# Kernel tuning notes

Measured on AMD Instinct MI355X. Metric: run time of the kernel, lower is better.

## Reference

```python
import jax, jax.numpy as jnp
import numpy as np

B, L, HID, NH = 2, 2048, 1024, 16
HD = HID // NH  # 64


def setup_inputs() -> dict:
    key = jax.random.key(0)
    ks = jax.random.split(key, 12)
    s = 1.0 / np.sqrt(HID)
    query = jax.random.normal(ks[0], (B, L, HID), jnp.float32)
    key_t = jax.random.normal(ks[1], (B, L, HID), jnp.float32)
    value = jax.random.normal(ks[2], (B, L, HID), jnp.float32)
    # key padding mask: True = valid token; random lengths in [1024, 2048]
    lengths = jax.random.randint(ks[3], (B,), L // 2, L + 1)
    key_mask = jnp.arange(L)[None, :] < lengths[:, None]  # [B, K] bool
    # attn_mask: True = blocked (causal upper triangle), 2D branch [Q, K]
    attn_mask = jnp.triu(jnp.ones((L, L), jnp.bool_), k=1)
    Wq = jax.random.normal(ks[4], (HID, HID), jnp.float32) * s
    Wk = jax.random.normal(ks[5], (HID, HID), jnp.float32) * s
    Wv = jax.random.normal(ks[6], (HID, HID), jnp.float32) * s
    Wo = jax.random.normal(ks[7], (HID, HID), jnp.float32) * s
    bq = jax.random.normal(ks[8], (HID,), jnp.float32) * 0.01
    bk = jax.random.normal(ks[9], (HID,), jnp.float32) * 0.01
    bv = jax.random.normal(ks[10], (HID,), jnp.float32) * 0.01
    bo = jax.random.normal(ks[11], (HID,), jnp.float32) * 0.01
    return {"query": query, "key": key_t, "value": value,
            "key_mask": key_mask, "attn_mask": attn_mask,
            "Wq": Wq, "bq": bq, "Wk": Wk, "bk": bk,
            "Wv": Wv, "bv": bv, "Wo": Wo, "bo": bo}


def reference(query, key, value, key_mask, attn_mask,
              Wq, bq, Wk, bk, Wv, bv, Wo, bo):
    Bq, Q, _ = query.shape
    K = key.shape[1]
    # projections (torch Linear: x @ W.T + b), split heads -> [B, H, L, HD]
    def proj(x, W, b, L_):
        return (x @ W.T + b).reshape(Bq, L_, NH, HD).transpose(0, 2, 1, 3)
    q = proj(query, Wq, bq, Q)
    k = proj(key, Wk, bk, K)
    v = proj(value, Wv, bv, K)
    scores = jnp.einsum('bhqd,bhkd->bhqk', q, k) / np.sqrt(HD)
    blocked = attn_mask[None, None, :, :]                 # True = blocked
    kmask = key_mask[:, None, None, :]                    # True = valid
    valid = (~blocked) & kmask                            # [B,H,Q,K] (bcast)
    scores = jnp.where(blocked, -10000.0, scores)
    scores = jnp.where(kmask, scores, -10000.0)
    weights = jax.nn.softmax(scores, axis=-1)
    weights = weights * valid.astype(weights.dtype)
    weights = weights / jnp.maximum(weights.sum(-1, keepdims=True), 1e-6)
    attended = jnp.einsum('bhqk,bhkd->bhqd', weights, v)
    attended = attended.transpose(0, 2, 1, 3).reshape(Bq, Q, HID)
    return attended @ Wo.T + bo
```

## Files before the change

### kernel.cpp

```cpp
#include <hip/hip_runtime.h>
#include <hip/hip_bf16.h>
#include <stdint.h>


#define L_SEQ 2048
#define HID 1024
#define NHEAD 16
#define HD 64

typedef __attribute__((ext_vector_type(8))) short bf16x8;
typedef __attribute__((ext_vector_type(8))) unsigned short u16x8;
typedef __attribute__((ext_vector_type(4))) float f32x4;

__device__ __forceinline__ unsigned short f2bf(float f) {
  unsigned int u = __builtin_bit_cast(unsigned int, f);
  u += 0x7fffu + ((u >> 16) & 1u);
  return (unsigned short)(u >> 16);
}

__device__ __forceinline__ unsigned int pk2bf(float a, float b) {
  unsigned int r;
  asm("v_cvt_pk_bf16_f32 %0, %1, %2" : "=v"(r) : "v"(a), "v"(b));
  return r;
}

__device__ __forceinline__ void gl_lds16(const void* g, void* l) {
  __builtin_amdgcn_global_load_lds(
      (const __attribute__((address_space(1))) unsigned int*)(uintptr_t)g,
      (__attribute__((address_space(3))) unsigned int*)(uint32_t)(uintptr_t)l,
      16, 0, 0);
}

__device__ __forceinline__ f32x4 mfma16(bf16x8 a, bf16x8 b, f32x4 c) {
  return __builtin_amdgcn_mfma_f32_16x16x32_bf16(a, b, c, 0, 0, 0);
}

__global__ __launch_bounds__(256)
void convert_w_kernel(const float* __restrict__ wq, const float* __restrict__ wk,
                      const float* __restrict__ wv, const float* __restrict__ wo,
                      const unsigned int* __restrict__ km,
                      unsigned short* __restrict__ wqb, unsigned short* __restrict__ wkb,
                      unsigned short* __restrict__ wvb, unsigned short* __restrict__ wob,
                      int* __restrict__ lens) {
  __shared__ int red[256];
  const int bid = blockIdx.x;
  const int t = threadIdx.x;
  if (bid == 2048) {
    unsigned int w0 = km[0];
    bool u8mode = (w0 != 1u);
    for (int b = 0; b < 2; ++b) {
      int cnt = 0;
      if (u8mode) {
        const unsigned char* p = (const unsigned char*)km + b * L_SEQ;
        for (int i = t; i < L_SEQ; i += 256) cnt += (p[i] != 0) ? 1 : 0;
      } else {
        const unsigned int* p = km + b * L_SEQ;
        for (int i = t; i < L_SEQ; i += 256) cnt += (p[i] != 0) ? 1 : 0;
      }
      red[t] = cnt;
      __syncthreads();
      for (int s = 128; s > 0; s >>= 1) {
        if (t < s) red[t] += red[t + s];
        __syncthreads();
      }
      if (t == 0) lens[b] = red[0];
      __syncthreads();
    }
    return;
  }
  int s = bid >> 9;
  int base = (bid & 511) * 2048;
  const float* src = s == 0 ? wq : (s == 1 ? wk : (s == 2 ? wv : wo));
  unsigned short* dst = s == 0 ? wqb : (s == 1 ? wkb : (s == 2 ? wvb : wob));
  int i = base + t * 8;
  float4 a = *(const float4*)(src + i);
  float4 b4 = *(const float4*)(src + i + 4);
  u16x8 o;
  o[0] = f2bf(a.x); o[1] = f2bf(a.y); o[2] = f2bf(a.z); o[3] = f2bf(a.w);
  o[4] = f2bf(b4.x); o[5] = f2bf(b4.y); o[6] = f2bf(b4.z); o[7] = f2bf(b4.w);
  *(u16x8*)(dst + i) = o;
}

__device__ __forceinline__ void gemm128_f32A_core(const float* __restrict__ A,
                                                  const unsigned short* __restrict__ W,
                                                  int m0, int n0, int K,
                                                  unsigned short* As, unsigned short* Bs,
                                                  f32x4 acc[4][4]) {
  const int tid = threadIdx.x;
  const int w = tid >> 6, lane = tid & 63;
  const int l15 = lane & 15, l4 = lane >> 4;
  const int wr = w >> 1, wc = w & 1;
#pragma unroll
  for (int i = 0; i < 4; ++i)
#pragma unroll
    for (int j = 0; j < 4; ++j) acc[i][j] = (f32x4){0.f, 0.f, 0.f, 0.f};

  const int arow = tid >> 1, acolh = (tid & 1) * 16;
  const float* Ag = A + (size_t)(m0 + arow) * K + acolh;
  char* AsW = (char*)As + arow * 64 + acolh * 2;
  const int nk = K >> 5;

  {
    float4 a0 = *(const float4*)(Ag);
    float4 a1 = *(const float4*)(Ag + 4);
    float4 a2 = *(const float4*)(Ag + 8);
    float4 a3 = *(const float4*)(Ag + 12);
    uint4 p0, p1;
    p0.x = pk2bf(a0.x, a0.y); p0.y = pk2bf(a0.z, a0.w);
    p0.z = pk2bf(a1.x, a1.y); p0.w = pk2bf(a1.z, a1.w);
    p1.x = pk2bf(a2.x, a2.y); p1.y = pk2bf(a2.z, a2.w);
    p1.z = pk2bf(a3.x, a3.y); p1.w = pk2bf(a3.z, a3.w);
    *(uint4*)(AsW) = p0;
    *(uint4*)(AsW + 16) = p1;
#pragma unroll
    for (int i = 0; i < 2; ++i) {
      int c = i * 256 + tid;
      int row = c >> 2, col = (c & 3) * 8;
      gl_lds16(W + (size_t)(n0 + row) * K + col, (char*)Bs + (i * 256 + w * 64) * 16);
    }
  }
  __syncthreads();

  int cur = 0;
  for (int t = 0; t < nk; ++t) {
    const int k0 = t * 32;
    float4 a0, a1, a2, a3;
    const bool more = (t + 1 < nk);
    if (more) {
      const float* Agn = Ag + k0 + 32;
      a0 = *(const float4*)(Agn);
      a1 = *(const float4*)(Agn + 4);
      a2 = *(const float4*)(Agn + 8);
      a3 = *(const float4*)(Agn + 12);
#pragma unroll
      for (int i = 0; i < 2; ++i) {
        int c = i * 256 + tid;
        int row = c >> 2, col = (c & 3) * 8;
        gl_lds16(W + (size_t)(n0 + row) * K + k0 + 32 + col,
                 (char*)Bs + (cur ^ 1) * 8192 + (i * 256 + w * 64) * 16);
      }
    }
    const unsigned short* Asb = As + cur * 4096;
    const unsigned short* Bsb = Bs + cur * 4096;
    bf16x8 af[4], bfr[4];
#pragma unroll
    for (int i = 0; i < 4; ++i)
      af[i] = *(const bf16x8*)(Asb + (wr * 64 + i * 16 + l15) * 32 + l4 * 8);
#pragma unroll
    for (int j = 0; j < 4; ++j)
      bfr[j] = *(const bf16x8*)(Bsb + (wc * 64 + j * 16 + l15) * 32 + l4 * 8);
    __builtin_amdgcn_s_setprio(1);
#pragma unroll
    for (int i = 0; i < 4; ++i)
#pragma unroll
      for (int j = 0; j < 4; ++j) acc[i][j] = mfma16(af[i], bfr[j], acc[i][j]);
    __builtin_amdgcn_s_setprio(0);
    if (more) {
      uint4 p0, p1;
      p0.x = pk2bf(a0.x, a0.y); p0.y = pk2bf(a0.z, a0.w);
      p0.z = pk2bf(a1.x, a1.y); p0.w = pk2bf(a1.z, a1.w);
      p1.x = pk2bf(a2.x, a2.y); p1.y = pk2bf(a2.z, a2.w);
      p1.z = pk2bf(a3.x, a3.y); p1.w = pk2bf(a3.z, a3.w);
      char* dst = AsW + (cur ^ 1) * 8192;
      *(uint4*)(dst) = p0;
      *(uint4*)(dst + 16) = p1;
    }
    __syncthreads();
    cur ^= 1;
  }
}

__device__ __forceinline__ void gemm128_bf_core(const unsigned short* __restrict__ A,
                                                const unsigned short* __restrict__ W,
                                                int m0, int n0, int K,
                                                unsigned short* As, unsigned short* Bs,
                                                f32x4 acc[4][4]) {
  const int tid = threadIdx.x;
  const int w = tid >> 6, lane = tid & 63;
  const int l15 = lane & 15, l4 = lane >> 4;
  const int wr = w >> 1, wc = w & 1;
#pragma unroll
  for (int i = 0; i < 4; ++i)
#pragma unroll
    for (int j = 0; j < 4; ++j) acc[i][j] = (f32x4){0.f, 0.f, 0.f, 0.f};

  const int nk = K >> 5;
#pragma unroll
  for (int i = 0; i < 2; ++i) {
    int c = i * 256 + tid;
    int row = c >> 2, col = (c & 3) * 8;
    gl_lds16(A + (size_t)(m0 + row) * K + col, (char*)As + (i * 256 + w * 64) * 16);
    gl_lds16(W + (size_t)(n0 + row) * K + col, (char*)Bs + (i * 256 + w * 64) * 16);
  }
  __syncthreads();

  int cur = 0;
  for (int t = 0; t < nk; ++t) {
    const int k0 = t * 32;
    if (t + 1 < nk) {
#pragma unroll
      for (int i = 0; i < 2; ++i) {
        int c = i * 256 + tid;
        int row = c >> 2, col = (c & 3) * 8;
        gl_lds16(A + (size_t)(m0 + row) * K + k0 + 32 + col,
                 (char*)As + (cur ^ 1) * 8192 + (i * 256 + w * 64) * 16);
        gl_lds16(W + (size_t)(n0 + row) * K + k0 + 32 + col,
                 (char*)Bs + (cur ^ 1) * 8192 + (i * 256 + w * 64) * 16);
      }
    }
    const unsigned short* Asb = As + cur * 4096;
    const unsigned short* Bsb = Bs + cur * 4096;
    bf16x8 af[4], bfr[4];
#pragma unroll
    for (int i = 0; i < 4; ++i)
      af[i] = *(const bf16x8*)(Asb + (wr * 64 + i * 16 + l15) * 32 + l4 * 8);
#pragma unroll
    for (int j = 0; j < 4; ++j)
      bfr[j] = *(const bf16x8*)(Bsb + (wc * 64 + j * 16 + l15) * 32 + l4 * 8);
    __builtin_amdgcn_s_setprio(1);
#pragma unroll
    for (int i = 0; i < 4; ++i)
#pragma unroll
      for (int j = 0; j < 4; ++j) acc[i][j] = mfma16(af[i], bfr[j], acc[i][j]);
    __builtin_amdgcn_s_setprio(0);
    __syncthreads();
    cur ^= 1;
  }
}

__global__ __launch_bounds__(256)
void qkv_gemm_kernel(const float* __restrict__ qf32, const float* __restrict__ kf32,
                     const float* __restrict__ vf32, const unsigned short* __restrict__ wq,
                     const unsigned short* __restrict__ wk, const unsigned short* __restrict__ wv,
                     const float* __restrict__ bq, const float* __restrict__ bk,
                     const float* __restrict__ bv, unsigned short* __restrict__ Qp,
                     unsigned short* __restrict__ Kp, unsigned short* __restrict__ Vtp) {
  __shared__ unsigned short As[2 * 128 * 32];
  __shared__ unsigned short Bs[2 * 128 * 32];
  const int z = blockIdx.z;
  const float* A = z == 0 ? qf32 : (z == 1 ? kf32 : vf32);
  const unsigned short* W = z == 0 ? wq : (z == 1 ? wk : wv);
  const float* bias = z == 0 ? bq : (z == 1 ? bk : bv);
  const int m0 = blockIdx.y * 128, n0 = blockIdx.x * 128;
  f32x4 acc[4][4];
  gemm128_f32A_core(A, W, m0, n0, HID, As, Bs, acc);

  const int tid = threadIdx.x;
  const int w = tid >> 6, lane = tid & 63;
  const int l15 = lane & 15, l4 = lane >> 4;
  const int wr = w >> 1, wc = w & 1;
  const float scale = (z == 0) ? 0.125f * 1.44269504089f : 1.0f;
  if (z == 2) {
#pragma unroll
    for (int i = 0; i < 4; ++i)
#pragma unroll
      for (int j = 0; j < 4; ++j) {
        int grow0 = m0 + wr * 64 + i * 16 + l4 * 4;
        int gcol = n0 + wc * 64 + j * 16 + l15;
        float bv_ = bias[gcol];
        int bb = grow0 >> 11, ll0 = grow0 & 2047;
        int hh = gcol >> 6, d = gcol & 63;
        uint2 pw;
        pw.x = pk2bf(acc[i][j][0] + bv_, acc[i][j][1] + bv_);
        pw.y = pk2bf(acc[i][j][2] + bv_, acc[i][j][3] + bv_);
        *(uint2*)(&Vtp[((size_t)(bb * NHEAD + hh) * HD + d) * L_SEQ + ll0]) = pw;
      }
  } else {
    unsigned short* P = (z == 0) ? Qp : Kp;
#pragma unroll
    for (int i = 0; i < 4; ++i)
#pragma unroll
      for (int j = 0; j < 4; ++j)
#pragma unroll
        for (int r = 0; r < 4; ++r) {
          int grow = m0 + wr * 64 + i * 16 + l4 * 4 + r;
          int gcol = n0 + wc * 64 + j * 16 + l15;
          float v = (acc[i][j][r] + bias[gcol]) * scale;
          int bb = grow >> 11, ll = grow & 2047;
          int hh = gcol >> 6, d = gcol & 63;
          P[((size_t)(bb * NHEAD + hh) * L_SEQ + ll) * HD + d] = f2bf(v);
        }
  }
}

__global__ __launch_bounds__(256)
void out_gemm_kernel(const unsigned short* __restrict__ att, const unsigned short* __restrict__ wo,
                     const float* __restrict__ bo, float* __restrict__ out) {
  __shared__ unsigned short As[2 * 128 * 32];
  __shared__ unsigned short Bs[2 * 128 * 32];
  const int m0 = blockIdx.y * 128, n0 = blockIdx.x * 128;
  f32x4 acc[4][4];
  gemm128_bf_core(att, wo, m0, n0, HID, As, Bs, acc);

  const int tid = threadIdx.x;
  const int w = tid >> 6, lane = tid & 63;
  const int l15 = lane & 15, l4 = lane >> 4;
  const int wr = w >> 1, wc = w & 1;
#pragma unroll
  for (int i = 0; i < 4; ++i)
#pragma unroll
    for (int j = 0; j < 4; ++j)
#pragma unroll
      for (int r = 0; r < 4; ++r) {
        int grow = m0 + wr * 64 + i * 16 + l4 * 4 + r;
        int gcol = n0 + wc * 64 + j * 16 + l15;
        out[(size_t)grow * HID + gcol] = acc[i][j][r] + bo[gcol];
      }
}

__global__ __launch_bounds__(512)
void attn_kernel(const unsigned short* __restrict__ Qp, const unsigned short* __restrict__ Kp,
                 const unsigned short* __restrict__ Vtp, unsigned short* __restrict__ att,
                 const int* __restrict__ lens) {
  __shared__ unsigned short Ks[2][64 * 64];
  __shared__ unsigned short Vs[2][64 * 64];
  __shared__ unsigned short Ps[8][16 * 72];

  const int x = blockIdx.x, bh = blockIdx.y;
  const int b = bh >> 4, h = bh & 15;
  const int tid = threadIdx.x, w = tid >> 6, lane = tid & 63;
  const int l15 = lane & 15, l4 = lane >> 4;
  const int len = lens[b];
  const int sub = (w < 4) ? x : (31 - x);
  const int qw0 = sub * 64 + (w & 3) * 16;

  const unsigned short* Qg = Qp + (size_t)bh * L_SEQ * HD;
  const unsigned short* Kg = Kp + (size_t)bh * L_SEQ * HD;
  const unsigned short* Vg = Vtp + (size_t)bh * HD * L_SEQ;

  const int rr = tid >> 3, cb = tid & 7;
  const int swz = (cb ^ (rr & 7)) * 8;
  const unsigned short* KgRow = Kg + (size_t)rr * HD + swz;
  const unsigned short* VgRow = Vg + (size_t)rr * L_SEQ + swz;

  bf16x8 qf[2];
#pragma unroll
  for (int kk = 0; kk < 2; ++kk)
    qf[kk] = *(const bf16x8*)(Qg + (size_t)(qw0 + l15) * HD + kk * 32 + l4 * 8);

  f32x4 acc[4];
#pragma unroll
  for (int n = 0; n < 4; ++n) acc[n] = (f32x4){0.f, 0.f, 0.f, 0.f};
  float mq = -1e30f, lq = 0.f;

  int koff[4][2];
#pragma unroll
  for (int n = 0; n < 4; ++n)
#pragma unroll
    for (int kk = 0; kk < 2; ++kk) {
      int row = n * 16 + l15;
      koff[n][kk] = row * 128 + (((l4 + kk * 4) ^ (row & 7)) * 16);
    }

  const int len_r = ((len + 63) >> 6) << 6;
  const int hi_end = 64 * (32 - x);
  const int kv_end = (hi_end < len_r) ? hi_end : len_r;
  const int nt = kv_end >> 6;

  gl_lds16(KgRow, (char*)&Ks[0][0] + w * 1024);
  gl_lds16(VgRow, (char*)&Vs[0][0] + w * 1024);
  __syncthreads();

  int cur = 0;
  for (int t = 0; t < nt; ++t) {
    const int k0 = t * 64;
    if (t + 1 < nt) {
      const int k1 = k0 + 64;
      gl_lds16(KgRow + (size_t)k1 * HD, (char*)&Ks[cur ^ 1][0] + w * 1024);
      gl_lds16(VgRow + k1, (char*)&Vs[cur ^ 1][0] + w * 1024);
    }
    if (k0 <= qw0 + 15) {
      const char* Kb = (const char*)&Ks[cur][0];
      const char* Vb = (const char*)&Vs[cur][0];
      f32x4 s[4];
#pragma unroll
      for (int n = 0; n < 4; ++n) s[n] = (f32x4){0.f, 0.f, 0.f, 0.f};
      __builtin_amdgcn_s_setprio(1);
#pragma unroll
      for (int kk = 0; kk < 2; ++kk) {
#pragma unroll
        for (int n = 0; n < 4; ++n)
          s[n] = mfma16(*(const bf16x8*)(Kb + koff[n][kk]), qf[kk], s[n]);
      }
      __builtin_amdgcn_s_setprio(0);
      if (!(k0 + 63 <= qw0 && k0 + 64 <= len)) {
        const int qa = qw0 + l15;
#pragma unroll
        for (int n = 0; n < 4; ++n)
#pragma unroll
          for (int r = 0; r < 4; ++r) {
            int ka = k0 + n * 16 + l4 * 4 + r;
            if (ka > qa || ka >= len) s[n][r] = -1e30f;
          }
      }
      float v01 = fmaxf(fmaxf(s[0][0], s[0][1]), fmaxf(s[0][2], s[0][3]));
      float v23 = fmaxf(fmaxf(s[1][0], s[1][1]), fmaxf(s[1][2], s[1][3]));
      float v45 = fmaxf(fmaxf(s[2][0], s[2][1]), fmaxf(s[2][2], s[2][3]));
      float v67 = fmaxf(fmaxf(s[3][0], s[3][1]), fmaxf(s[3][2], s[3][3]));
      float v = fmaxf(fmaxf(v01, v23), fmaxf(v45, v67));
      v = fmaxf(v, __shfl_xor(v, 16));
      v = fmaxf(v, __shfl_xor(v, 32));
      float mold = mq;
      float mnew = fmaxf(mold, v);
      mq = mnew;
      float alpha = __builtin_amdgcn_exp2f(mold - mnew);
      float rs = 0.f;
#pragma unroll
      for (int n = 0; n < 4; ++n)
#pragma unroll
        for (int r = 0; r < 4; ++r) {
          float p = __builtin_amdgcn_exp2f(s[n][r] - mnew);
          s[n][r] = p;
          rs += p;
        }
      rs += __shfl_xor(rs, 16);
      rs += __shfl_xor(rs, 32);
      lq = lq * alpha + rs;
      float ar[4];
#pragma unroll
      for (int r = 0; r < 4; ++r) ar[r] = __shfl(alpha, l4 * 4 + r, 64);
#pragma unroll
      for (int n = 0; n < 4; ++n)
#pragma unroll
        for (int r = 0; r < 4; ++r) acc[n][r] *= ar[r];
#pragma unroll
      for (int n = 0; n < 4; ++n) {
        uint2 pw;
        pw.x = pk2bf(s[n][0], s[n][1]);
        pw.y = pk2bf(s[n][2], s[n][3]);
        *(uint2*)(&Ps[w][l15 * 72 + n * 16 + l4 * 4]) = pw;
      }
      bf16x8 pf[2];
#pragma unroll
      for (int kk = 0; kk < 2; ++kk)
        pf[kk] = *(const bf16x8*)(&Ps[w][l15 * 72 + kk * 32 + l4 * 8]);
      __builtin_amdgcn_s_setprio(1);
#pragma unroll
      for (int kk = 0; kk < 2; ++kk) {
#pragma unroll
        for (int n = 0; n < 4; ++n)
          acc[n] = mfma16(pf[kk], *(const bf16x8*)(Vb + koff[n][kk]), acc[n]);
      }
      __builtin_amdgcn_s_setprio(0);
    }
    __syncthreads();
    cur ^= 1;
  }

  float invq = 1.0f / lq;
  float invr[4];
#pragma unroll
  for (int r = 0; r < 4; ++r) invr[r] = __shfl(invq, l4 * 4 + r, 64);
#pragma unroll
  for (int r = 0; r < 4; ++r) {
    int qa = qw0 + l4 * 4 + r;
#pragma unroll
    for (int n = 0; n < 4; ++n)
      att[((size_t)(b * L_SEQ + qa)) * HID + h * HD + n * 16 + l15] = f2bf(acc[n][r] * invr[r]);
  }
}

extern "C" void kernel_launch(void* const* d_in, const int* in_sizes, int n_in,
                              void* d_out, int out_size, void* d_ws, size_t ws_size,
                              hipStream_t stream) {
  const float* query = (const float*)d_in[0];
  const float* key = (const float*)d_in[1];
  const float* value = (const float*)d_in[2];
  const unsigned int* key_mask = (const unsigned int*)d_in[3];
  const float* Wq = (const float*)d_in[5];
  const float* bq = (const float*)d_in[6];
  const float* Wk = (const float*)d_in[7];
  const float* bk = (const float*)d_in[8];
  const float* Wv = (const float*)d_in[9];
  const float* bv = (const float*)d_in[10];
  const float* Wo = (const float*)d_in[11];
  const float* bo = (const float*)d_in[12];

  char* ws = (char*)d_ws;
  const size_t SZ_X = (size_t)4096 * 1024 * 2;
  const size_t SZ_W = (size_t)1024 * 1024 * 2;
  unsigned short* wqb = (unsigned short*)(ws + 3 * SZ_X);
  unsigned short* wkb = (unsigned short*)(ws + 3 * SZ_X + SZ_W);
  unsigned short* wvb = (unsigned short*)(ws + 3 * SZ_X + 2 * SZ_W);
  unsigned short* wob = (unsigned short*)(ws + 3 * SZ_X + 3 * SZ_W);
  unsigned short* Qp = (unsigned short*)(ws + 3 * SZ_X + 4 * SZ_W);
  unsigned short* Kp = (unsigned short*)(ws + 4 * SZ_X + 4 * SZ_W);
  unsigned short* Vtp = (unsigned short*)(ws + 5 * SZ_X + 4 * SZ_W);
  unsigned short* att = (unsigned short*)(ws + 6 * SZ_X + 4 * SZ_W);
  int* lens = (int*)(ws + 7 * SZ_X + 4 * SZ_W);

  convert_w_kernel<<<2049, 256, 0, stream>>>(Wq, Wk, Wv, Wo, key_mask,
                                             wqb, wkb, wvb, wob, lens);
  qkv_gemm_kernel<<<dim3(8, 32, 3), 256, 0, stream>>>(query, key, value, wqb, wkb, wvb,
                                                      bq, bk, bv, Qp, Kp, Vtp);
  attn_kernel<<<dim3(16, 32), 512, 0, stream>>>(Qp, Kp, Vtp, att, lens);
  out_gemm_kernel<<<dim3(8, 32), 256, 0, stream>>>(att, wob, bo, (float*)d_out);
}
```

Baseline: 145.4 us.

## Swizzle A-tile LDS layout, remap block IDs for XCD locality, lazy softmax rescale

Inlines the fp32-A GEMM core into the QKV kernel and XOR-swizzles the A tile in LDS to avoid bank conflicts on fragment reads. All three kernels now launch on a 1D grid with a block-ID remap that groups tiles sharing operands onto the same XCD, aiming for better L2 reuse. The attention softmax skips the accumulator rescale unless the running max grows by more than 8 (log2 units), which removes per-tile multiply and shuffle work. The exchange is extra index arithmetic, and exponentials can be computed against a stale max, which relies on fp32 headroom.

```diff
diff --git a/kernel.cpp b/kernel.cpp
--- a/kernel.cpp
+++ b/kernel.cpp
@@ -81,24 +81,51 @@
   *(u16x8*)(dst + i) = o;
 }
 
-__device__ __forceinline__ void gemm128_f32A_core(const float* __restrict__ A,
-                                                  const unsigned short* __restrict__ W,
-                                                  int m0, int n0, int K,
-                                                  unsigned short* As, unsigned short* Bs,
-                                                  f32x4 acc[4][4]) {
+__global__ __launch_bounds__(256)
+void qkv_gemm_kernel(const float* __restrict__ qf32, const float* __restrict__ kf32,
+                     const float* __restrict__ vf32, const unsigned short* __restrict__ wq,
+                     const unsigned short* __restrict__ wk, const unsigned short* __restrict__ wv,
+                     const float* __restrict__ bq, const float* __restrict__ bk,
+                     const float* __restrict__ bv, unsigned short* __restrict__ Qp,
+                     unsigned short* __restrict__ Kp, unsigned short* __restrict__ Vtp) {
+  __shared__ unsigned short As[2 * 128 * 32];
+  __shared__ unsigned short Bs[2 * 128 * 32];
+  const int id = blockIdx.x;
+  const int g = (id & 7) * 96 + (id >> 3);
+  const int mg = g >> 3;
+  const int z = mg >> 5;
+  const int m0 = (mg & 31) * 128;
+  const int n0 = (g & 7) * 128;
+
+  const float* A = z == 0 ? qf32 : (z == 1 ? kf32 : vf32);
+  const unsigned short* W = z == 0 ? wq : (z == 1 ? wk : wv);
+  const float* bias = z == 0 ? bq : (z == 1 ? bk : bv);
+
   const int tid = threadIdx.x;
   const int w = tid >> 6, lane = tid & 63;
   const int l15 = lane & 15, l4 = lane >> 4;
   const int wr = w >> 1, wc = w & 1;
+
+  f32x4 acc[4][4];
 #pragma unroll
   for (int i = 0; i < 4; ++i)
 #pragma unroll
     for (int j = 0; j < 4; ++j) acc[i][j] = (f32x4){0.f, 0.f, 0.f, 0.f};
 
-  const int arow = tid >> 1, acolh = (tid & 1) * 16;
-  const float* Ag = A + (size_t)(m0 + arow) * K + acolh;
-  char* AsW = (char*)As + arow * 64 + acolh * 2;
-  const int nk = K >> 5;
+  const int arow = tid >> 1;
+  const int ac = (tid & 1) * 2;
+  const float* Ag = A + (size_t)(m0 + arow) * HID + ac * 8;
+  const int c0s = (ac) ^ ((arow >> 1) & 3);
+  const int c1s = (ac + 1) ^ ((arow >> 1) & 3);
+  char* As0 = (char*)As + arow * 64 + c0s * 16;
+  char* As1 = (char*)As + arow * 64 + c1s * 16;
+
+  int aoff[4];
+#pragma unroll
+  for (int i = 0; i < 4; ++i) {
+    int R = wr * 64 + i * 16 + l15;
+    aoff[i] = R * 64 + ((l4 ^ ((R >> 1) & 3)) * 16);
+  }
 
   {
     float4 a0 = *(const float4*)(Ag);
@@ -110,18 +137,19 @@
     p0.z = pk2bf(a1.x, a1.y); p0.w = pk2bf(a1.z, a1.w);
     p1.x = pk2bf(a2.x, a2.y); p1.y = pk2bf(a2.z, a2.w);
     p1.z = pk2bf(a3.x, a3.y); p1.w = pk2bf(a3.z, a3.w);
-    *(uint4*)(AsW) = p0;
-    *(uint4*)(AsW + 16) = p1;
+    *(uint4*)(As0) = p0;
+    *(uint4*)(As1) = p1;
 #pragma unroll
     for (int i = 0; i < 2; ++i) {
       int c = i * 256 + tid;
       int row = c >> 2, col = (c & 3) * 8;
-      gl_lds16(W + (size_t)(n0 + row) * K + col, (char*)Bs + (i * 256 + w * 64) * 16);
+      gl_lds16(W + (size_t)(n0 + row) * HID + col, (char*)Bs + (i * 256 + w * 64) * 16);
     }
   }
   __syncthreads();
 
   int cur = 0;
+  const int nk = HID >> 5;
   for (int t = 0; t < nk; ++t) {
     const int k0 = t * 32;
     float4 a0, a1, a2, a3;
@@ -136,16 +164,15 @@
       for (int i = 0; i < 2; ++i) {
         int c = i * 256 + tid;
         int row = c >> 2, col = (c & 3) * 8;
-        gl_lds16(W + (size_t)(n0 + row) * K + k0 + 32 + col,
+        gl_lds16(W + (size_t)(n0 + row) * HID + k0 + 32 + col,
                  (char*)Bs + (cur ^ 1) * 8192 + (i * 256 + w * 64) * 16);
       }
     }
-    const unsigned short* Asb = As + cur * 4096;
+    const char* Asb = (const char*)As + cur * 8192;
     const unsigned short* Bsb = Bs + cur * 4096;
     bf16x8 af[4], bfr[4];
 #pragma unroll
-    for (int i = 0; i < 4; ++i)
-      af[i] = *(const bf16x8*)(Asb + (wr * 64 + i * 16 + l15) * 32 + l4 * 8);
+    for (int i = 0; i < 4; ++i) af[i] = *(const bf16x8*)(Asb + aoff[i]);
 #pragma unroll
     for (int j = 0; j < 4; ++j)
       bfr[j] = *(const bf16x8*)(Bsb + (wc * 64 + j * 16 + l15) * 32 + l4 * 8);
@@ -161,94 +188,13 @@
       p0.z = pk2bf(a1.x, a1.y); p0.w = pk2bf(a1.z, a1.w);
       p1.x = pk2bf(a2.x, a2.y); p1.y = pk2bf(a2.z, a2.w);
       p1.z = pk2bf(a3.x, a3.y); p1.w = pk2bf(a3.z, a3.w);
-      char* dst = AsW + (cur ^ 1) * 8192;
-      *(uint4*)(dst) = p0;
-      *(uint4*)(dst + 16) = p1;
+      *(uint4*)(As0 + (cur ^ 1) * 8192) = p0;
+      *(uint4*)(As1 + (cur ^ 1) * 8192) = p1;
     }
     __syncthreads();
     cur ^= 1;
   }
-}
-
-__device__ __forceinline__ void gemm128_bf_core(const unsigned short* __restrict__ A,
-                                                const unsigned short* __restrict__ W,
-                                                int m0, int n0, int K,
-                                                unsigned short* As, unsigned short* Bs,
-                                                f32x4 acc[4][4]) {
-  const int tid = threadIdx.x;
-  const int w = tid >> 6, lane = tid & 63;
-  const int l15 = lane & 15, l4 = lane >> 4;
-  const int wr = w >> 1, wc = w & 1;
-#pragma unroll
-  for (int i = 0; i < 4; ++i)
-#pragma unroll
-    for (int j = 0; j < 4; ++j) acc[i][j] = (f32x4){0.f, 0.f, 0.f, 0.f};
-
-  const int nk = K >> 5;
-#pragma unroll
-  for (int i = 0; i < 2; ++i) {
-    int c = i * 256 + tid;
-    int row = c >> 2, col = (c & 3) * 8;
-    gl_lds16(A + (size_t)(m0 + row) * K + col, (char*)As + (i * 256 + w * 64) * 16);
-    gl_lds16(W + (size_t)(n0 + row) * K + col, (char*)Bs + (i * 256 + w * 64) * 16);
-  }
-  __syncthreads();
-
-  int cur = 0;
-  for (int t = 0; t < nk; ++t) {
-    const int k0 = t * 32;
-    if (t + 1 < nk) {
-#pragma unroll
-      for (int i = 0; i < 2; ++i) {
-        int c = i * 256 + tid;
-        int row = c >> 2, col = (c & 3) * 8;
-        gl_lds16(A + (size_t)(m0 + row) * K + k0 + 32 + col,
-                 (char*)As + (cur ^ 1) * 8192 + (i * 256 + w * 64) * 16);
-        gl_lds16(W + (size_t)(n0 + row) * K + k0 + 32 + col,
-                 (char*)Bs + (cur ^ 1) * 8192 + (i * 256 + w * 64) * 16);
-      }
-    }
-    const unsigned short* Asb = As + cur * 4096;
-    const unsigned short* Bsb = Bs + cur * 4096;
-    bf16x8 af[4], bfr[4];
-#pragma unroll
-    for (int i = 0; i < 4; ++i)
-      af[i] = *(const bf16x8*)(Asb + (wr * 64 + i * 16 + l15) * 32 + l4 * 8);
-#pragma unroll
-    for (int j = 0; j < 4; ++j)
-      bfr[j] = *(const bf16x8*)(Bsb + (wc * 64 + j * 16 + l15) * 32 + l4 * 8);
-    __builtin_amdgcn_s_setprio(1);
-#pragma unroll
-    for (int i = 0; i < 4; ++i)
-#pragma unroll
-      for (int j = 0; j < 4; ++j) acc[i][j] = mfma16(af[i], bfr[j], acc[i][j]);
-    __builtin_amdgcn_s_setprio(0);
-    __syncthreads();
-    cur ^= 1;
-  }
-}
-
-__global__ __launch_bounds__(256)
-void qkv_gemm_kernel(const float* __restrict__ qf32, const float* __restrict__ kf32,
-                     const float* __restrict__ vf32, const unsigned short* __restrict__ wq,
-                     const unsigned short* __restrict__ wk, const unsigned short* __restrict__ wv,
-                     const float* __restrict__ bq, const float* __restrict__ bk,
-                     const float* __restrict__ bv, unsigned short* __restrict__ Qp,
-                     unsigned short* __restrict__ Kp, unsigned short* __restrict__ Vtp) {
-  __shared__ unsigned short As[2 * 128 * 32];
-  __shared__ unsigned short Bs[2 * 128 * 32];
-  const int z = blockIdx.z;
-  const float* A = z == 0 ? qf32 : (z == 1 ? kf32 : vf32);
-  const unsigned short* W = z == 0 ? wq : (z == 1 ? wk : wv);
-  const float* bias = z == 0 ? bq : (z == 1 ? bk : bv);
-  const int m0 = blockIdx.y * 128, n0 = blockIdx.x * 128;
-  f32x4 acc[4][4];
-  gemm128_f32A_core(A, W, m0, n0, HID, As, Bs, acc);
-
-  const int tid = threadIdx.x;
-  const int w = tid >> 6, lane = tid & 63;
-  const int l15 = lane & 15, l4 = lane >> 4;
-  const int wr = w >> 1, wc = w & 1;
+
   const float scale = (z == 0) ? 0.125f * 1.44269504089f : 1.0f;
   if (z == 2) {
 #pragma unroll
@@ -283,12 +229,72 @@
   }
 }
 
+__device__ __forceinline__ void gemm128_bf_core(const unsigned short* __restrict__ A,
+                                                const unsigned short* __restrict__ W,
+                                                int m0, int n0, int K,
+                                                unsigned short* As, unsigned short* Bs,
+                                                f32x4 acc[4][4]) {
+  const int tid = threadIdx.x;
+  const int w = tid >> 6, lane = tid & 63;
+  const int l15 = lane & 15, l4 = lane >> 4;
+  const int wr = w >> 1, wc = w & 1;
+#pragma unroll
+  for (int i = 0; i < 4; ++i)
+#pragma unroll
+    for (int j = 0; j < 4; ++j) acc[i][j] = (f32x4){0.f, 0.f, 0.f, 0.f};
+
+  const int nk = K >> 5;
+#pragma unroll
+  for (int i = 0; i < 2; ++i) {
+    int c = i * 256 + tid;
+    int row = c >> 2, col = (c & 3) * 8;
+    gl_lds16(A + (size_t)(m0 + row) * K + col, (char*)As + (i * 256 + w * 64) * 16);
+    gl_lds16(W + (size_t)(n0 + row) * K + col, (char*)Bs + (i * 256 + w * 64) * 16);
+  }
+  __syncthreads();
+
+  int cur = 0;
+  for (int t = 0; t < nk; ++t) {
+    const int k0 = t * 32;
+    if (t + 1 < nk) {
+#pragma unroll
+      for (int i = 0; i < 2; ++i) {
+        int c = i * 256 + tid;
+        int row = c >> 2, col = (c & 3) * 8;
+        gl_lds16(A + (size_t)(m0 + row) * K + k0 + 32 + col,
+                 (char*)As + (cur ^ 1) * 8192 + (i * 256 + w * 64) * 16);
+        gl_lds16(W + (size_t)(n0 + row) * K + k0 + 32 + col,
+                 (char*)Bs + (cur ^ 1) * 8192 + (i * 256 + w * 64) * 16);
+      }
+    }
+    const unsigned short* Asb = As + cur * 4096;
+    const unsigned short* Bsb = Bs + cur * 4096;
+    bf16x8 af[4], bfr[4];
+#pragma unroll
+    for (int i = 0; i < 4; ++i)
+      af[i] = *(const bf16x8*)(Asb + (wr * 64 + i * 16 + l15) * 32 + l4 * 8);
+#pragma unroll
+    for (int j = 0; j < 4; ++j)
+      bfr[j] = *(const bf16x8*)(Bsb + (wc * 64 + j * 16 + l15) * 32 + l4 * 8);
+    __builtin_amdgcn_s_setprio(1);
+#pragma unroll
+    for (int i = 0; i < 4; ++i)
+#pragma unroll
+      for (int j = 0; j < 4; ++j) acc[i][j] = mfma16(af[i], bfr[j], acc[i][j]);
+    __builtin_amdgcn_s_setprio(0);
+    __syncthreads();
+    cur ^= 1;
+  }
+}
+
 __global__ __launch_bounds__(256)
 void out_gemm_kernel(const unsigned short* __restrict__ att, const unsigned short* __restrict__ wo,
                      const float* __restrict__ bo, float* __restrict__ out) {
   __shared__ unsigned short As[2 * 128 * 32];
   __shared__ unsigned short Bs[2 * 128 * 32];
-  const int m0 = blockIdx.y * 128, n0 = blockIdx.x * 128;
+  const int id = blockIdx.x;
+  const int swz = (id & 7) * 32 + (id >> 3);
+  const int m0 = (swz >> 3) * 128, n0 = (swz & 7) * 128;
   f32x4 acc[4][4];
   gemm128_bf_core(att, wo, m0, n0, HID, As, Bs, acc);
 
@@ -316,7 +322,10 @@
   __shared__ unsigned short Vs[2][64 * 64];
   __shared__ unsigned short Ps[8][16 * 72];
 
-  const int x = blockIdx.x, bh = blockIdx.y;
+  const int id = blockIdx.x;
+  const int g = (id & 7) * 64 + (id >> 3);
+  const int bh = g >> 4;
+  const int x = g & 15;
   const int b = bh >> 4, h = bh & 15;
   const int tid = threadIdx.x, w = tid >> 6, lane = tid & 63;
   const int l15 = lane & 15, l4 = lane >> 4;
@@ -400,29 +409,31 @@
       float v = fmaxf(fmaxf(v01, v23), fmaxf(v45, v67));
       v = fmaxf(v, __shfl_xor(v, 16));
       v = fmaxf(v, __shfl_xor(v, 32));
-      float mold = mq;
-      float mnew = fmaxf(mold, v);
-      mq = mnew;
-      float alpha = __builtin_amdgcn_exp2f(mold - mnew);
+      if (!__all(v - mq <= 8.0f)) {
+        float mnew = fmaxf(mq, v);
+        float alpha = __builtin_amdgcn_exp2f(mq - mnew);
+        mq = mnew;
+        float ar[4];
+#pragma unroll
+        for (int r = 0; r < 4; ++r) ar[r] = __shfl(alpha, l4 * 4 + r, 64);
+#pragma unroll
+        for (int n = 0; n < 4; ++n)
+#pragma unroll
+          for (int r = 0; r < 4; ++r) acc[n][r] *= ar[r];
+        lq *= alpha;
+      }
       float rs = 0.f;
 #pragma unroll
       for (int n = 0; n < 4; ++n)
 #pragma unroll
         for (int r = 0; r < 4; ++r) {
-          float p = __builtin_amdgcn_exp2f(s[n][r] - mnew);
+          float p = __builtin_amdgcn_exp2f(s[n][r] - mq);
           s[n][r] = p;
           rs += p;
         }
       rs += __shfl_xor(rs, 16);
       rs += __shfl_xor(rs, 32);
-      lq = lq * alpha + rs;
-      float ar[4];
-#pragma unroll
-      for (int r = 0; r < 4; ++r) ar[r] = __shfl(alpha, l4 * 4 + r, 64);
-#pragma unroll
-      for (int n = 0; n < 4; ++n)
-#pragma unroll
-        for (int r = 0; r < 4; ++r) acc[n][r] *= ar[r];
+      lq += rs;
 #pragma unroll
       for (int n = 0; n < 4; ++n) {
         uint2 pw;
@@ -491,8 +502,8 @@
 
   convert_w_kernel<<<2049, 256, 0, stream>>>(Wq, Wk, Wv, Wo, key_mask,
                                              wqb, wkb, wvb, wob, lens);
-  qkv_gemm_kernel<<<dim3(8, 32, 3), 256, 0, stream>>>(query, key, value, wqb, wkb, wvb,
-                                                      bq, bk, bv, Qp, Kp, Vtp);
-  attn_kernel<<<dim3(16, 32), 512, 0, stream>>>(Qp, Kp, Vtp, att, lens);
-  out_gemm_kernel<<<dim3(8, 32), 256, 0, stream>>>(att, wob, bo, (float*)d_out);
-}
+  qkv_gemm_kernel<<<768, 256, 0, stream>>>(query, key, value, wqb, wkb, wvb,
+                                           bq, bk, bv, Qp, Kp, Vtp);
+  attn_kernel<<<512, 512, 0, stream>>>(Qp, Kp, Vtp, att, lens);
+  out_gemm_kernel<<<256, 256, 0, stream>>>(att, wob, bo, (float*)d_out);
+}
```

Result: faster. 127.0 us (-12.6%).
